# Performance work log

Measured on AMD Instinct MI355X. Metric: run time of the kernel, lower is better.

The kernel has to match this reference:

```python
import jax, jax.numpy as jnp
import numpy as np

OUT = 14      # RoIAlign output size
RATIO = 2     # sampling ratio per bin
NMS_THR = 0.5


def _pairwise_iou(b):
    # b: [N,4] xyxy
    x1, y1, x2, y2 = b[:, 0], b[:, 1], b[:, 2], b[:, 3]
    area = (x2 - x1) * (y2 - y1)
    ix1 = jnp.maximum(x1[:, None], x1[None, :])
    iy1 = jnp.maximum(y1[:, None], y1[None, :])
    ix2 = jnp.minimum(x2[:, None], x2[None, :])
    iy2 = jnp.minimum(y2[:, None], y2[None, :])
    inter = jnp.clip(ix2 - ix1, 0.0) * jnp.clip(iy2 - iy1, 0.0)
    return inter / (area[:, None] + area[None, :] - inter + 1e-9)


def _nms(verts, scores, level, thr):
    # greedy NMS restricted to boxes assigned to the same FPN level
    N = verts.shape[0]
    order = jnp.argsort(-scores)
    bs, ls = verts[order], level[order]
    iou = _pairwise_iou(bs)
    idx = jnp.arange(N)
    sup_mat = (iou > thr) & (ls[:, None] == ls[None, :]) & (idx[None, :] > idx[:, None])
    def body(i, keep):
        return keep & ~(sup_mat[i] & keep[i])
    keep_s = jax.lax.fori_loop(0, N, body, jnp.ones((N,), dtype=bool))
    return jnp.zeros((N,), dtype=bool).at[order].set(keep_s)


def _roi_align(feat, rois):
    # feat: [C,H,W]; rois: [N,4] xyxy in feature-map coords
    C, H, W = feat.shape
    N = rois.shape[0]
    S = OUT * RATIO
    x1, y1, x2, y2 = rois[:, 0], rois[:, 1], rois[:, 2], rois[:, 3]
    bw = (x2 - x1) / OUT
    bh = (y2 - y1) / OUT
    g = (jnp.arange(S, dtype=feat.dtype) + 0.5) / RATIO  # sample grid in bin units
    sx = x1[:, None] + g[None, :] * bw[:, None]           # [N,S]
    sy = y1[:, None] + g[None, :] * bh[:, None]
    xs = jnp.broadcast_to(jnp.clip(sx, 0.0, W - 1.0)[:, None, :], (N, S, S))
    ys = jnp.broadcast_to(jnp.clip(sy, 0.0, H - 1.0)[:, :, None], (N, S, S))
    x0 = jnp.floor(xs); y0 = jnp.floor(ys)
    x0i = x0.astype(jnp.int32); y0i = y0.astype(jnp.int32)
    x1i = jnp.minimum(x0i + 1, W - 1)
    y1i = jnp.minimum(y0i + 1, H - 1)
    lx = xs - x0; ly = ys - y0
    flat = feat.reshape(C, H * W)
    def gather(yi, xi):
        return jnp.take(flat, (yi * W + xi).reshape(-1), axis=1).reshape(C, N, S, S)
    v = (gather(y0i, x0i) * (1 - ly) * (1 - lx)
         + gather(y0i, x1i) * (1 - ly) * lx
         + gather(y1i, x0i) * ly * (1 - lx)
         + gather(y1i, x1i) * ly * lx)
    # average the RATIO x RATIO samples per output bin
    v = v.reshape(C, N, OUT, RATIO, OUT, RATIO).mean(axis=(3, 5))
    return jnp.transpose(v, (1, 0, 2, 3))  # [N,C,14,14]


def reference(p4, p8, p16, p32, boxes, scores):
    # boxes: [B,N,4] (cx,cy,w,h) in image coords; scores: [B,N]
    w, h = boxes[..., 2], boxes[..., 3]
    # FPN level assignment: clamp(floor(3 + log2(sqrt(w*h)/224)), 1, 4)
    level = jnp.clip(jnp.floor(3.0 + jnp.log2(jnp.sqrt(w * h) / 224.0)), 1.0, 4.0)
    cx, cy = boxes[..., 0], boxes[..., 1]
    verts = jnp.stack([cx - w / 2, cy - h / 2, cx + w / 2, cy + h / 2], axis=-1)
    keep = jax.vmap(lambda v, s, l: _nms(v, s, l, NMS_THR))(verts, scores, level)
    feats = {1: p4, 2: p8, 3: p16, 4: p32}
    pooled = jnp.zeros(boxes.shape[:2] + (p4.shape[1], OUT, OUT), dtype=p4.dtype)
    for l in (1, 2, 3, 4):
        stride = float(2 * 2 ** l)  # 4/8/16/32, matches prepare_boxes
        p = jax.vmap(_roi_align)(feats[l], verts / stride)  # [B,N,C,14,14]
        sel = ((level == l) & keep)[:, :, None, None, None]
        pooled = pooled + jnp.where(sel, p, 0.0)
    out_boxes = jnp.where(keep[..., None], verts, 0.0)
    return pooled, out_boxes, keep


def setup_inputs() -> dict:
    key = jax.random.key(0)
    ks = jax.random.split(key, 7)
    B, N, C = 2, 512, 256
    p4 = jax.random.normal(ks[0], (B, C, 256, 256), jnp.float32)
    p8 = jax.random.normal(ks[1], (B, C, 128, 128), jnp.float32)
    p16 = jax.random.normal(ks[2], (B, C, 64, 64), jnp.float32)
    p32 = jax.random.normal(ks[3], (B, C, 32, 32), jnp.float32)
    cxcy = jax.random.uniform(ks[4], (B, N, 2), jnp.float32) * 1024.0
    wh = 16.0 + jax.random.uniform(ks[5], (B, N, 2), jnp.float32) * 496.0
    boxes = jnp.concatenate([cxcy, wh], axis=-1)
    scores = jax.random.uniform(ks[6], (B, N), jnp.float32)
    return {"p4": p4, "p8": p8, "p16": p16, "p32": p32, "boxes": boxes, "scores": scores}
```

## Files before the change

kernel.cpp:

```cpp
#include <hip/hip_runtime.h>

#define NB 2
#define NN 512
#define NC 256
#define OUTP 14
#define SS 28
#define CH_SPLIT 4
#define CH_PER_BLK (NC / CH_SPLIT)
#define ELEMS_PER_BLK (CH_PER_BLK * OUTP * OUTP)
#define POOL_PER_BOX (NC * OUTP * OUTP)
#define POOL_TOTAL (NB * NN * POOL_PER_BOX)
#define BOX_OFF POOL_TOTAL
#define KEEP_OFF (POOL_TOTAL + NB * NN * 4)

#define GCH 4
#define NGRP (CH_PER_BLK / GCH)
#define PATCH_MAX 1256

typedef const __attribute__((address_space(1))) unsigned int GU32;
typedef __attribute__((address_space(3))) unsigned int LU32;

__global__ __launch_bounds__(512) void k_nms(const float* __restrict__ boxes,
                                             const float* __restrict__ scores,
                                             float* __restrict__ dout) {
    int b = blockIdx.x;
    int tid = threadIdx.x;
    __shared__ float sS[NN];
    __shared__ int sI[NN];
    __shared__ float4 sB[NN];
    __shared__ float sA[NN];
    __shared__ int sL[NN];
    __shared__ unsigned long long sup[NN][8];
    __shared__ unsigned long long skw[8];
    __shared__ int korig[NN];

    sS[tid] = scores[b * NN + tid];
    sI[tid] = tid;
    __syncthreads();
    for (int k = 2; k <= NN; k <<= 1) {
        for (int j = k >> 1; j > 0; j >>= 1) {
            int ixj = tid ^ j;
            if (ixj > tid) {
                float s1 = sS[tid], s2 = sS[ixj];
                int i1 = sI[tid], i2 = sI[ixj];
                bool lt = (s1 > s2) || (s1 == s2 && i1 < i2);
                bool up = ((tid & k) == 0);
                if (up ? !lt : lt) {
                    sS[tid] = s2; sS[ixj] = s1;
                    sI[tid] = i2; sI[ixj] = i1;
                }
            }
            __syncthreads();
        }
    }
    {
        int o = sI[tid];
        float4 bx = ((const float4*)boxes)[b * NN + o];
        float w = bx.z, h = bx.w;
        float x1 = bx.x - w * 0.5f, y1 = bx.y - h * 0.5f;
        float x2 = bx.x + w * 0.5f, y2 = bx.y + h * 0.5f;
        float s = sqrtf(w * h);
        int lvl = (s < 112.f) ? 1 : ((s < 224.f) ? 2 : ((s < 448.f) ? 3 : 4));
        sB[tid] = make_float4(x1, y1, x2, y2);
        sA[tid] = (x2 - x1) * (y2 - y1);
        sL[tid] = lvl;
    }
    __syncthreads();
    {
        float4 bi = sB[tid];
        float areai = sA[tid];
        int il = sL[tid];
        for (int cg = 0; cg < 8; ++cg) {
            unsigned long long m = 0ull;
            int jb = cg << 6;
#pragma unroll 4
            for (int k = 0; k < 64; ++k) {
                int j = jb + k;
                float4 bj = sB[j];
                float xx1 = fmaxf(bi.x, bj.x);
                float yy1 = fmaxf(bi.y, bj.y);
                float xx2 = fminf(bi.z, bj.z);
                float yy2 = fminf(bi.w, bj.w);
                float inter = fmaxf(xx2 - xx1, 0.0f) * fmaxf(yy2 - yy1, 0.0f);
                float denom = areai + sA[j] - inter + 1e-9f;
                bool sp = (j > tid) && (sL[j] == il) && ((inter / denom) > 0.5f);
                m |= sp ? (1ull << k) : 0ull;
            }
            sup[tid][cg] = m;
        }
    }
    __syncthreads();
    if (tid < 64) {
        int myw = tid & 7;
        unsigned long long kwl = ~0ull;
        for (int w = 0; w < 8; ++w) {
            unsigned long long aw = __shfl(kwl, w);
            int ibase = w << 6;
            for (int bb = 0; bb < 64; ++bb) {
                int i = ibase + bb;
                unsigned long long rw = sup[i][w];
                unsigned long long rl = sup[i][myw];
                if ((aw >> bb) & 1ull) {
                    aw &= ~rw;
                    kwl &= ~rl;
                }
            }
        }
        if (tid < 8) skw[tid] = kwl;
    }
    __syncthreads();
    korig[sI[tid]] = (int)((skw[tid >> 6] >> (tid & 63)) & 1ull);
    __syncthreads();
    {
        float4 bx = ((const float4*)boxes)[b * NN + tid];
        float kf = korig[tid] ? 1.0f : 0.0f;
        float x1 = (bx.x - bx.z * 0.5f) * kf;
        float y1 = (bx.y - bx.w * 0.5f) * kf;
        float x2 = (bx.x + bx.z * 0.5f) * kf;
        float y2 = (bx.y + bx.w * 0.5f) * kf;
        ((float4*)(dout + BOX_OFF))[b * NN + tid] = make_float4(x1, y1, x2, y2);
        dout[KEEP_OFF + b * NN + tid] = kf;
    }
}

__global__ __launch_bounds__(256, 4) void k_roi(const float* __restrict__ p4,
                                                const float* __restrict__ p8,
                                                const float* __restrict__ p16,
                                                const float* __restrict__ p32,
                                                const float* __restrict__ boxes,
                                                float* __restrict__ dout) {
    int blk = blockIdx.x;
    int box = blk >> 2;
    int chunk = blk & 3;
    int b = box >> 9;
    int tid = threadIdx.x;
    float* obase = dout + (size_t)box * POOL_PER_BOX + (size_t)chunk * ELEMS_PER_BLK;
    float keepf = dout[KEEP_OFF + box];
    if (keepf < 0.5f) {
        float4 z = make_float4(0.f, 0.f, 0.f, 0.f);
        float4* o4 = (float4*)obase;
        for (int i = tid; i < ELEMS_PER_BLK / 4; i += 256) o4[i] = z;
        return;
    }
    float4 bx = ((const float4*)boxes)[box];
    float w = bx.z, h = bx.w;
    float s = sqrtf(w * h);
    int lvl = (s < 112.f) ? 0 : ((s < 224.f) ? 1 : ((s < 448.f) ? 2 : 3));
    const float* feat = (lvl == 0) ? p4 : ((lvl == 1) ? p8 : ((lvl == 2) ? p16 : p32));
    int HW = 256 >> lvl;
    float inv = 1.0f / (float)(4 << lvl);
    int planesz = HW * HW;
    const float* plane0 = feat + (size_t)b * NC * planesz + (size_t)(chunk * CH_PER_BLK) * planesz;

    float x1r = (bx.x - w * 0.5f) * inv;
    float bwr = w * inv / 14.0f;
    float y1r = (bx.y - h * 0.5f) * inv;
    float bhr = h * inv / 14.0f;
    float hwm1 = (float)(HW - 1);
    float xs_first = fminf(fmaxf(x1r + 0.25f * bwr, 0.0f), hwm1);
    float xs_last  = fminf(fmaxf(x1r + 13.75f * bwr, 0.0f), hwm1);
    float ys_first = fminf(fmaxf(y1r + 0.25f * bhr, 0.0f), hwm1);
    float ys_last  = fminf(fmaxf(y1r + 13.75f * bhr, 0.0f), hwm1);
    int x_lo = min((int)floorf(xs_first), HW - 2);
    int x_hi = min((int)floorf(xs_last) + 1, HW - 1);
    int y_lo = min((int)floorf(ys_first), HW - 2);
    int y_hi = min((int)floorf(ys_last) + 1, HW - 1);
    int PW = x_hi - x_lo + 1;
    int PH = y_hi - y_lo + 1;
    int cells = PW * PH;
    int cm1 = cells - 1;
    float invPW = 1.0f / (float)PW;
    int I = (cells + 255) >> 8;

    __shared__ float patch[2][GCH * PATCH_MAX];
    __shared__ int sXc0[SS], sYoff[SS];
    __shared__ float sLX[SS], sLY[SS];

    if (tid < SS) {
        float g = (tid + 0.5f) * 0.5f;
        float xs = fminf(fmaxf(x1r + g * bwr, 0.0f), hwm1);
        int x0 = min((int)floorf(xs), HW - 2);
        sXc0[tid] = x0 - x_lo;
        sLX[tid] = xs - (float)x0;
        float ys = fminf(fmaxf(y1r + g * bhr, 0.0f), hwm1);
        int y0 = min((int)floorf(ys), HW - 2);
        sYoff[tid] = (y0 - y_lo) * PW;
        sLY[tid] = ys - (float)y0;
    }

    const int base_gidx = y_lo * HW + x_lo;

#define STAGE(gidx, bufi)                                                                   \
    do {                                                                                    \
        const float* plg_ = plane0 + (size_t)((gidx) * GCH) * planesz + base_gidx;          \
        for (int k_ = 0; k_ < I; ++k_) {                                                    \
            int i_ = tid + (k_ << 8);                                                       \
            int iq_ = min(i_, cm1);                                                         \
            int row_ = (int)(((float)iq_ + 0.5f) * invPW);                                  \
            int voff_ = row_ * (HW - PW) + iq_;        \
            _Pragma("unroll")                                                               \
            for (int c_ = 0; c_ < GCH; ++c_) {                                              \
                __builtin_amdgcn_global_load_lds(                                           \
                    (GU32*)(plg_ + (size_t)c_ * planesz + voff_),                           \
                    (LU32*)(&patch[bufi][c_ * PATCH_MAX] + i_), 4, 0, 0);                   \
            }                                                                               \
        }                                                                                   \
    } while (0)

    STAGE(0, 0);

    for (int g = 0; g < NGRP; ++g) {
        if (g + 1 < NGRP) {
            STAGE(g + 1, (g + 1) & 1);
            switch (I) {
                case 1:  asm volatile("s_waitcnt vmcnt(4) lgkmcnt(0)" ::: "memory"); break;
                case 2:  asm volatile("s_waitcnt vmcnt(8) lgkmcnt(0)" ::: "memory"); break;
                case 3:  asm volatile("s_waitcnt vmcnt(12) lgkmcnt(0)" ::: "memory"); break;
                default: asm volatile("s_waitcnt vmcnt(16) lgkmcnt(0)" ::: "memory"); break;
            }
        } else {
            asm volatile("s_waitcnt vmcnt(0) lgkmcnt(0)" ::: "memory");
        }
        __builtin_amdgcn_s_barrier();
        asm volatile("" ::: "memory");

        const float* Pb = &patch[g & 1][0];
        float* obg = obase + g * (GCH * 196);
        for (int idx = tid; idx < GCH * 196; idx += 256) {
            int c = idx / 196;
            int p = idx - c * 196;
            int py = p / 14;
            int px = p - py * 14;
            const float* P = Pb + c * PATCH_MAX;
            int ix = px << 1, iy = py << 1;
            int ro0 = sYoff[iy],  ro1 = sYoff[iy + 1];
            float ly0 = sLY[iy],  ly1 = sLY[iy + 1];
            int c00 = sXc0[ix],   c01 = sXc0[ix + 1];
            float lx0 = sLX[ix],  lx1 = sLX[ix + 1];
            float acc = 0.f;
#define SAMPLE(RO, LY, CC, LX)                                        \
            {                                                         \
                const float* q_ = P + (RO) + (CC);                    \
                float f00 = q_[0], f01 = q_[1];                       \
                const float* q2_ = q_ + PW;                           \
                float f10 = q2_[0], f11 = q2_[1];                     \
                float top = f00 + (LX) * (f01 - f00);                 \
                float bot = f10 + (LX) * (f11 - f10);                 \
                acc += top + (LY) * (bot - top);                      \
            }
            SAMPLE(ro0, ly0, c00, lx0)
            SAMPLE(ro0, ly0, c01, lx1)
            SAMPLE(ro1, ly1, c00, lx0)
            SAMPLE(ro1, ly1, c01, lx1)
#undef SAMPLE
            obg[idx] = acc * 0.25f;
        }

        if (g + 1 < NGRP) {
            asm volatile("" ::: "memory");
            __builtin_amdgcn_s_barrier();
            asm volatile("" ::: "memory");
        }
    }
#undef STAGE
}

extern "C" void kernel_launch(void* const* d_in, const int* in_sizes, int n_in,
                              void* d_out, int out_size, void* d_ws, size_t ws_size,
                              hipStream_t stream) {
    const float* p4 = (const float*)d_in[0];
    const float* p8 = (const float*)d_in[1];
    const float* p16 = (const float*)d_in[2];
    const float* p32 = (const float*)d_in[3];
    const float* boxes = (const float*)d_in[4];
    const float* scores = (const float*)d_in[5];
    float* out = (float*)d_out;

    k_nms<<<NB, NN, 0, stream>>>(boxes, scores, out);
    k_roi<<<NB * NN * CH_SPLIT, 256, 0, stream>>>(p4, p8, p16, p32, boxes, out);
}
```

Before: 536.3 us.

## Give each wavefront its own channels and double-buffered LDS patch without block barriers

Each of the four wavefronts in a block now owns 16 channels and stages one channel patch at a time into its own double-buffered LDS region. Waits use per-wave vmcnt instead of block-wide barriers, so waves run independently. Each lane also computes two adjacent outputs and writes them as a float2. The change removes barrier stalls and gives wider stores, at the cost of more sequential load iterations per wave when patches are large. The launch-bounds occupancy hint of 4 is dropped.

New measurement: 539.7 us. About the same (+0.6%).

```diff
diff --git a/kernel.cpp b/kernel.cpp
--- a/kernel.cpp
+++ b/kernel.cpp
@@ -13,8 +13,7 @@
 #define BOX_OFF POOL_TOTAL
 #define KEEP_OFF (POOL_TOTAL + NB * NN * 4)
 
-#define GCH 4
-#define NGRP (CH_PER_BLK / GCH)
+#define CPW 16
 #define PATCH_MAX 1256
 
 typedef const __attribute__((address_space(1))) unsigned int GU32;
@@ -123,12 +122,12 @@
     }
 }
 
-__global__ __launch_bounds__(256, 4) void k_roi(const float* __restrict__ p4,
-                                                const float* __restrict__ p8,
-                                                const float* __restrict__ p16,
-                                                const float* __restrict__ p32,
-                                                const float* __restrict__ boxes,
-                                                float* __restrict__ dout) {
+__global__ __launch_bounds__(256) void k_roi(const float* __restrict__ p4,
+                                             const float* __restrict__ p8,
+                                             const float* __restrict__ p16,
+                                             const float* __restrict__ p32,
+                                             const float* __restrict__ boxes,
+                                             float* __restrict__ dout) {
     int blk = blockIdx.x;
     int box = blk >> 2;
     int chunk = blk & 3;
@@ -170,9 +169,9 @@
     int cells = PW * PH;
     int cm1 = cells - 1;
     float invPW = 1.0f / (float)PW;
-    int I = (cells + 255) >> 8;
-
-    __shared__ float patch[2][GCH * PATCH_MAX];
+    int I64 = (cells + 63) >> 6;
+
+    __shared__ float patch[4][2][PATCH_MAX];
     __shared__ int sXc0[SS], sYoff[SS];
     __shared__ float sLX[SS], sLY[SS];
 
@@ -187,82 +186,98 @@
         sYoff[tid] = (y0 - y_lo) * PW;
         sLY[tid] = ys - (float)y0;
     }
-
+    __syncthreads();
+
+    int wid = tid >> 6;
+    int lane = tid & 63;
     const int base_gidx = y_lo * HW + x_lo;
-
-#define STAGE(gidx, bufi)                                                                   \
+    const float* wplane = plane0 + (size_t)(wid * CPW) * planesz + base_gidx;
+    float* wout = obase + (size_t)(wid * CPW) * 196;
+    LU32* wlds0 = (LU32*)&patch[wid][0][0];
+    LU32* wlds1 = (LU32*)&patch[wid][1][0];
+
+#define STAGE(j, ldsp)                                                                      \
     do {                                                                                    \
-        const float* plg_ = plane0 + (size_t)((gidx) * GCH) * planesz + base_gidx;          \
-        for (int k_ = 0; k_ < I; ++k_) {                                                    \
-            int i_ = tid + (k_ << 8);                                                       \
+        const float* pl_ = wplane + (size_t)(j) * planesz;                                  \
+        for (int k_ = 0; k_ < I64; ++k_) {                                                  \
+            int i_ = lane + (k_ << 6);                                                      \
             int iq_ = min(i_, cm1);                                                         \
             int row_ = (int)(((float)iq_ + 0.5f) * invPW);                                  \
-            int voff_ = row_ * (HW - PW) + iq_;        \
-            _Pragma("unroll")                                                               \
-            for (int c_ = 0; c_ < GCH; ++c_) {                                              \
-                __builtin_amdgcn_global_load_lds(                                           \
-                    (GU32*)(plg_ + (size_t)c_ * planesz + voff_),                           \
-                    (LU32*)(&patch[bufi][c_ * PATCH_MAX] + i_), 4, 0, 0);                   \
-            }                                                                               \
+            int voff_ = row_ * (HW - PW) + iq_;                           \
+            __builtin_amdgcn_global_load_lds((GU32*)(pl_ + voff_), (ldsp) + i_, 4, 0, 0);   \
         }                                                                                   \
     } while (0)
 
-    STAGE(0, 0);
-
-    for (int g = 0; g < NGRP; ++g) {
-        if (g + 1 < NGRP) {
-            STAGE(g + 1, (g + 1) & 1);
-            switch (I) {
-                case 1:  asm volatile("s_waitcnt vmcnt(4) lgkmcnt(0)" ::: "memory"); break;
-                case 2:  asm volatile("s_waitcnt vmcnt(8) lgkmcnt(0)" ::: "memory"); break;
-                case 3:  asm volatile("s_waitcnt vmcnt(12) lgkmcnt(0)" ::: "memory"); break;
-                default: asm volatile("s_waitcnt vmcnt(16) lgkmcnt(0)" ::: "memory"); break;
+#define VMCNT(N) asm volatile("s_waitcnt vmcnt(" #N ")" ::: "memory")
+
+    STAGE(0, wlds0);
+
+    for (int j = 0; j < CPW; ++j) {
+        if (j + 1 < CPW) {
+            STAGE(j + 1, (j & 1) ? wlds0 : wlds1);
+            switch (I64) {
+                case 1:  VMCNT(1);  break;
+                case 2:  VMCNT(2);  break;
+                case 3:  VMCNT(3);  break;
+                case 4:  VMCNT(4);  break;
+                case 5:  VMCNT(5);  break;
+                case 6:  VMCNT(6);  break;
+                case 7:  VMCNT(7);  break;
+                case 8:  VMCNT(8);  break;
+                case 9:  VMCNT(9);  break;
+                case 10: VMCNT(10); break;
+                case 11: VMCNT(11); break;
+                case 12: VMCNT(12); break;
+                case 13: VMCNT(13); break;
+                case 14: VMCNT(14); break;
+                case 15: VMCNT(15); break;
+                default: VMCNT(16); break;
             }
         } else {
-            asm volatile("s_waitcnt vmcnt(0) lgkmcnt(0)" ::: "memory");
-        }
-        __builtin_amdgcn_s_barrier();
-        asm volatile("" ::: "memory");
-
-        const float* Pb = &patch[g & 1][0];
-        float* obg = obase + g * (GCH * 196);
-        for (int idx = tid; idx < GCH * 196; idx += 256) {
-            int c = idx / 196;
-            int p = idx - c * 196;
-            int py = p / 14;
-            int px = p - py * 14;
-            const float* P = Pb + c * PATCH_MAX;
-            int ix = px << 1, iy = py << 1;
-            int ro0 = sYoff[iy],  ro1 = sYoff[iy + 1];
-            float ly0 = sLY[iy],  ly1 = sLY[iy + 1];
-            int c00 = sXc0[ix],   c01 = sXc0[ix + 1];
-            float lx0 = sLX[ix],  lx1 = sLX[ix + 1];
-            float acc = 0.f;
+            VMCNT(0);
+        }
+
+        const float* P = &patch[wid][j & 1][0];
+        float* oc = wout + j * 196;
+#pragma unroll
+        for (int it = 0; it < 2; ++it) {
+            int p0 = (lane << 1) + (it << 7);
+            if (p0 < 196) {
+                int py = p0 / 14;
+                int px = p0 - py * 14;
+                int iy = py << 1;
+                int ro0 = sYoff[iy],  ro1 = sYoff[iy + 1];
+                float ly0 = sLY[iy],  ly1 = sLY[iy + 1];
+                float2 r;
+#pragma unroll
+                for (int q = 0; q < 2; ++q) {
+                    int ix = (px + q) << 1;
+                    int c00 = sXc0[ix],   c01 = sXc0[ix + 1];
+                    float lx0 = sLX[ix],  lx1 = sLX[ix + 1];
+                    float acc = 0.f;
 #define SAMPLE(RO, LY, CC, LX)                                        \
-            {                                                         \
-                const float* q_ = P + (RO) + (CC);                    \
-                float f00 = q_[0], f01 = q_[1];                       \
-                const float* q2_ = q_ + PW;                           \
-                float f10 = q2_[0], f11 = q2_[1];                     \
-                float top = f00 + (LX) * (f01 - f00);                 \
-                float bot = f10 + (LX) * (f11 - f10);                 \
-                acc += top + (LY) * (bot - top);                      \
-            }
-            SAMPLE(ro0, ly0, c00, lx0)
-            SAMPLE(ro0, ly0, c01, lx1)
-            SAMPLE(ro1, ly1, c00, lx0)
-            SAMPLE(ro1, ly1, c01, lx1)
+                    {                                                 \
+                        const float* q_ = P + (RO) + (CC);            \
+                        float f00 = q_[0], f01 = q_[1];               \
+                        const float* q2_ = q_ + PW;                   \
+                        float f10 = q2_[0], f11 = q2_[1];             \
+                        float top = f00 + (LX) * (f01 - f00);         \
+                        float bot = f10 + (LX) * (f11 - f10);         \
+                        acc += top + (LY) * (bot - top);              \
+                    }
+                    SAMPLE(ro0, ly0, c00, lx0)
+                    SAMPLE(ro0, ly0, c01, lx1)
+                    SAMPLE(ro1, ly1, c00, lx0)
+                    SAMPLE(ro1, ly1, c01, lx1)
 #undef SAMPLE
-            obg[idx] = acc * 0.25f;
-        }
-
-        if (g + 1 < NGRP) {
-            asm volatile("" ::: "memory");
-            __builtin_amdgcn_s_barrier();
-            asm volatile("" ::: "memory");
+                    if (q == 0) r.x = acc * 0.25f; else r.y = acc * 0.25f;
+                }
+                *(float2*)(oc + p0) = r;
+            }
         }
     }
 #undef STAGE
+#undef VMCNT
 }
 
 extern "C" void kernel_launch(void* const* d_in, const int* in_sizes, int n_in,
```
